# Kernel tuning notes

Measured on AMD Instinct MI355X. Metric: run time of the kernel, lower is better.

## Reference

```python
import jax, jax.numpy as jnp
import numpy as np

ROBOT_W = 1.0
PHASE_W = 1.0
COHER_W = 10.0
SPEED_W = 5.0
MAX_SPEED = 10.0
SMOOTH_VEL_W = 0.05
SMOOTH_ACC_W = 0.01

# illegal phase transitions {(0,2),(1,0),(2,0),(2,1)} as a 3x3 lookup table
_ILLEGAL = np.zeros((3, 3), dtype=bool)
for a, b in [(0, 2), (1, 0), (2, 0), (2, 1)]:
    _ILLEGAL[a, b] = True
ILLEGAL_TABLE = jnp.asarray(_ILLEGAL)


def setup_inputs() -> dict:
    key = jax.random.key(0)
    k1, k2, k3, k4 = jax.random.split(key, 4)
    B, T = 256, 8192
    # scale by 8 so per-frame speeds (norm of diffs of 3-vectors) exceed MAX_SPEED
    pred_robot = jax.random.normal(k1, (B, T, 12), dtype=jnp.float32) * 8.0
    gt_robot = jax.random.normal(k2, (B, T, 12), dtype=jnp.float32) * 8.0
    pred_phase = jax.random.normal(k3, (B, T, 3), dtype=jnp.float32)
    gt_phase = jax.random.randint(k4, (B, T), 0, 3, dtype=jnp.int32)
    return {"pred_robot": pred_robot, "pred_phase": pred_phase,
            "gt_robot": gt_robot, "gt_phase": gt_phase}


def _coherence_loss(phase_logits):
    # vectorized replacement for the O(B*T) Python double loop
    p = jnp.argmax(phase_logits, axis=-1)            # [B, T]
    pt, pt1 = p[:, :-1], p[:, 1:]                    # [B, T-1]
    illegal = ILLEGAL_TABLE[pt, pt1]                 # [B, T-1] bool
    # logit of the (illegal) predicted phase at t+1
    sel = jnp.take_along_axis(phase_logits[:, 1:], pt1[..., None], axis=-1)[..., 0]
    loss_sum = jnp.sum(jnp.where(illegal, sel * sel, 0.0))
    count = jnp.sum(illegal)
    return jnp.where(count > 0, loss_sum / jnp.maximum(count, 1).astype(sel.dtype), 0.0)


def _speed_loss(pred_robot):
    B, T, D = pred_robot.shape
    vel = pred_robot[:, 1:] - pred_robot[:, :-1]     # [B, T-1, 12]
    pts = vel.reshape(B, T - 1, 4, 3)
    speeds = jnp.linalg.norm(pts, axis=-1)           # [B, T-1, 4]
    pen = jax.nn.relu(speeds - MAX_SPEED)
    return SPEED_W * jnp.mean(pen * pen)


def reference(pred_robot, pred_phase, gt_robot, gt_phase):
    # MSE over robot trajectory
    robot_loss = jnp.mean((pred_robot - gt_robot) ** 2)
    # cross-entropy over 3 phase classes
    logp = jax.nn.log_softmax(pred_phase, axis=-1)   # [B, T, 3]
    nll = -jnp.take_along_axis(logp, gt_phase[..., None].astype(jnp.int32), axis=-1)[..., 0]
    phase_loss = jnp.mean(nll)
    coherence = _coherence_loss(pred_phase)
    speed_loss = _speed_loss(pred_robot)
    vel = pred_robot[:, 1:] - pred_robot[:, :-1]
    vel_loss = jnp.mean(vel * vel)
    acc = pred_robot[:, 2:] - 2.0 * pred_robot[:, 1:-1] + pred_robot[:, :-2]
    acc_loss = jnp.mean(acc * acc)
    total = (ROBOT_W * robot_loss + PHASE_W * phase_loss + COHER_W * coherence
             + speed_loss + SMOOTH_VEL_W * vel_loss + SMOOTH_ACC_W * acc_loss)
    return total
```

## Files before the change

kernel.cpp:

```cpp
#include <hip/hip_runtime.h>
#include <math.h>

#define B_DIM 256
#define T_DIM 8192
#define BLOCK 256
#define ITERS 4
#define RB_BLOCKS 6144
#define PH_BLOCKS 1536
#define GRID_BLOCKS (RB_BLOCKS + PH_BLOCKS)
#define NSLOT 256
#define N4_ROBOT (B_DIM * T_DIM * 3)
#define N4_PHASE (B_DIM * T_DIM * 3 / 4)
#define BF4_ROBOT (T_DIM * 3)
#define BF4_PHASE (T_DIM * 3 / 4)


__global__ __launch_bounds__(BLOCK) void combined_loss_main(
    const float4* __restrict__ pred4,
    const float*  __restrict__ pred_phase,
    const float4* __restrict__ gt4,
    const int*    __restrict__ gt_phase,
    double* __restrict__ ws)
{
    __shared__ float s_red[4][8];
    const int tid = threadIdx.x;
    const int bx  = (int)blockIdx.x;

    float sse=0.f, nll=0.f, csum=0.f, ccnt=0.f, pen2=0.f, velsq=0.f, accsq=0.f;

    if (bx < RB_BLOCKS) {
        const int Jbase = bx * (BLOCK * ITERS);
        const int jbase = (bx % 24) * (BLOCK * ITERS);
        #pragma unroll
        for (int it = 0; it < ITERS; ++it) {
            const int o = it * BLOCK + tid;
            const int J = Jbase + o;
            const int j = jbase + o;

            float4 p0 = pred4[J];
            float4 g  = gt4[J];
            float4 p1 = pred4[min(J + 1, N4_ROBOT - 1)];
            float4 p3 = pred4[min(J + 3, N4_ROBOT - 1)];
            float4 p4 = pred4[min(J + 4, N4_ROBOT - 1)];
            float4 p6 = pred4[min(J + 6, N4_ROBOT - 1)];

            float d;
            d = p0.x - g.x; sse += d*d;  d = p0.y - g.y; sse += d*d;
            d = p0.z - g.z; sse += d*d;  d = p0.w - g.w; sse += d*d;

            const bool vv = j < (BF4_ROBOT - 3);
            const bool va = j < (BF4_ROBOT - 6);

            const float vx = p3.x - p0.x, vy = p3.y - p0.y;
            const float vz = p3.z - p0.z, vw = p3.w - p0.w;
            if (vv) velsq += vx*vx + vy*vy + vz*vz + vw*vw;

            if (va) {
                const float ax = p6.x - 2.f*p3.x + p0.x;
                const float ay = p6.y - 2.f*p3.y + p0.y;
                const float az = p6.z - 2.f*p3.z + p0.z;
                const float aw = p6.w - 2.f*p3.w + p0.w;
                accsq += ax*ax + ay*ay + az*az + aw*aw;
            }

            const float wx = p4.x - p1.x, wy = p4.y - p1.y;
            const int s3 = j % 3;
            const float c0x = (s3 == 0) ? vx : ((s3 == 1) ? vz : vy);
            const float c0y = (s3 == 0) ? vy : ((s3 == 1) ? vw : vz);
            const float c0z = (s3 == 0) ? vz : ((s3 == 1) ? wx : vw);
            if (vv) {
                const float sp0 = sqrtf(c0x*c0x + c0y*c0y + c0z*c0z);
                const float d0 = sp0 - 10.f;
                if (d0 > 0.f) pen2 += d0*d0;
                if (s3 == 0) {
                    const float sp1 = sqrtf(vw*vw + wx*wx + wy*wy);
                    const float d1 = sp1 - 10.f;
                    if (d1 > 0.f) pen2 += d1*d1;
                }
            }
        }
    } else {
        const int pb    = bx - RB_BLOCKS;
        const int batch = pb / 6;
        const int Mbase = pb * (BLOCK * ITERS);
        const int mbase = (pb % 6) * (BLOCK * ITERS);
        const int bT    = batch * T_DIM;
        const float4* ph4 = (const float4*)pred_phase;
        #pragma unroll
        for (int it = 0; it < ITERS; ++it) {
            const int o = it * BLOCK + tid;
            const int M = Mbase + o;
            const int m = mbase + o;

            float4 v  = ph4[M];
            float4 nv = ph4[min(M + 1, N4_PHASE - 1)];
            float4 nn = ph4[min(M + 2, N4_PHASE - 1)];

            const int q = m / 3;
            const int s = m - 3 * q;

            const int   rA  = 4*q + ((s == 0) ? 0 : ((s == 1) ? 2 : 3));
            const float la0 = (s == 0) ? v.x  : ((s == 1) ? v.z  : v.y);
            const float la1 = (s == 0) ? v.y  : ((s == 1) ? v.w  : v.z);
            const float la2 = (s == 0) ? v.z  : ((s == 1) ? nv.x : v.w);
            const float na0 = (s == 0) ? v.w  : ((s == 1) ? nv.y : nv.x);
            const float na1 = (s == 0) ? nv.x : ((s == 1) ? nv.z : nv.y);
            const float na2 = (s == 0) ? nv.y : ((s == 1) ? nv.w : nv.z);

            const int gA = gt_phase[bT + rA];
            {
                const float mx  = fmaxf(la0, fmaxf(la1, la2));
                const float lse = mx + logf(expf(la0-mx) + expf(la1-mx) + expf(la2-mx));
                const float sl  = (gA == 0) ? la0 : ((gA == 1) ? la1 : la2);
                nll += lse - sl;
            }
            if (rA < T_DIM - 1) {
                int p = 0; float pm = la0;
                if (la1 > pm) { pm = la1; p = 1; }
                if (la2 > pm) { pm = la2; p = 2; }
                int p1 = 0; float m1 = na0;
                if (na1 > m1) { m1 = na1; p1 = 1; }
                if (na2 > m1) { m1 = na2; p1 = 2; }
                const int mask = (p == 0) ? 4 : ((p == 1) ? 1 : 3);
                if ((mask >> p1) & 1) { csum += m1*m1; ccnt += 1.f; }
            }

            if (s == 0) {
                const int   rB  = 4*q + 1;
                const float lb0 = v.w,  lb1 = nv.x, lb2 = nv.y;
                const float nb0 = nv.z, nb1 = nv.w, nb2 = nn.x;
                const int gB = gt_phase[bT + rB];
                const float mx  = fmaxf(lb0, fmaxf(lb1, lb2));
                const float lse = mx + logf(expf(lb0-mx) + expf(lb1-mx) + expf(lb2-mx));
                const float sl  = (gB == 0) ? lb0 : ((gB == 1) ? lb1 : lb2);
                nll += lse - sl;
                int p = 0; float pm = lb0;
                if (lb1 > pm) { pm = lb1; p = 1; }
                if (lb2 > pm) { pm = lb2; p = 2; }
                int p1 = 0; float m1 = nb0;
                if (nb1 > m1) { m1 = nb1; p1 = 1; }
                if (nb2 > m1) { m1 = nb2; p1 = 2; }
                const int mask = (p == 0) ? 4 : ((p == 1) ? 1 : 3);
                if ((mask >> p1) & 1) { csum += m1*m1; ccnt += 1.f; }
            }
        }
    }

    float vals[7] = { sse, nll, csum, ccnt, pen2, velsq, accsq };
    #pragma unroll
    for (int off = 32; off > 0; off >>= 1) {
        #pragma unroll
        for (int q = 0; q < 7; ++q)
            vals[q] += __shfl_down(vals[q], off, 64);
    }
    const int wave = tid >> 6, lane = tid & 63;
    if (lane == 0) {
        #pragma unroll
        for (int q = 0; q < 7; ++q) s_red[wave][q] = vals[q];
    }
    __syncthreads();
    if (tid < 7) {
        double acc = (double)s_red[0][tid] + (double)s_red[1][tid]
                   + (double)s_red[2][tid] + (double)s_red[3][tid];
        atomicAdd(&ws[(size_t)(bx & (NSLOT - 1)) * 8 + tid], acc);
    }
}

__global__ __launch_bounds__(256) void combined_loss_final(
    const double* __restrict__ ws, float* __restrict__ out)
{
    __shared__ double sred[4][7];
    const int tid = threadIdx.x;
    double v[7];
    #pragma unroll
    for (int q = 0; q < 7; ++q) v[q] = ws[(size_t)tid * 8 + q];
    #pragma unroll
    for (int off = 32; off > 0; off >>= 1) {
        #pragma unroll
        for (int q = 0; q < 7; ++q)
            v[q] += __shfl_down(v[q], off, 64);
    }
    const int wave = tid >> 6, lane = tid & 63;
    if (lane == 0) {
        #pragma unroll
        for (int q = 0; q < 7; ++q) sred[wave][q] = v[q];
    }
    __syncthreads();
    if (tid == 0) {
        double s[7];
        #pragma unroll
        for (int q = 0; q < 7; ++q)
            s[q] = sred[0][q] + sred[1][q] + sred[2][q] + sred[3][q];
        const double robot = s[0] / (double)((size_t)B_DIM * T_DIM * 12);
        const double phase = s[1] / (double)((size_t)B_DIM * T_DIM);
        const double coher = (s[3] > 0.0) ? (s[2] / fmax(s[3], 1.0)) : 0.0;
        const double speed = 5.0  * (s[4] / (double)((size_t)B_DIM * (T_DIM - 1) * 4));
        const double vel   = 0.05 * (s[5] / (double)((size_t)B_DIM * (T_DIM - 1) * 12));
        const double acc   = 0.01 * (s[6] / (double)((size_t)B_DIM * (T_DIM - 2) * 12));
        out[0] = (float)(robot + phase + 10.0 * coher + speed + vel + acc);
    }
}

extern "C" void kernel_launch(void* const* d_in, const int* in_sizes, int n_in,
                              void* d_out, int out_size, void* d_ws, size_t ws_size,
                              hipStream_t stream)
{
    const float4* pred4      = (const float4*)d_in[0];
    const float*  pred_phase = (const float*)d_in[1];
    const float4* gt4        = (const float4*)d_in[2];
    const int*    gt_phase   = (const int*)d_in[3];
    double* ws  = (double*)d_ws;
    float*  out = (float*)d_out;

    hipMemsetAsync(d_ws, 0, (size_t)NSLOT * 8 * sizeof(double), stream);

    combined_loss_main<<<dim3(GRID_BLOCKS), BLOCK, 0, stream>>>(pred4, pred_phase, gt4, gt_phase, ws);
    combined_loss_final<<<1, 256, 0, stream>>>(ws, out);
}
```

Measured before the change: 241.1 us.

## Give each thread four contiguous float4s and reuse neighbor loads from registers

Each thread now handles four consecutive float4 elements instead of four elements strided by the block size. It loads a sliding window of 10 (robot) or 6 (phase) float4s once and reuses them across the four iterations, replacing 24 or 12 separate neighbor loads. The gt_phase loads are also hoisted ahead of the compute. The catch is that neighboring lanes now access addresses 64 bytes apart, so loads are no longer coalesced across a wavefront, and register pressure rises.

```diff
diff --git a/kernel.cpp b/kernel.cpp
--- a/kernel.cpp
+++ b/kernel.cpp
@@ -4,7 +4,6 @@
 #define B_DIM 256
 #define T_DIM 8192
 #define BLOCK 256
-#define ITERS 4
 #define RB_BLOCKS 6144
 #define PH_BLOCKS 1536
 #define GRID_BLOCKS (RB_BLOCKS + PH_BLOCKS)
@@ -12,7 +11,6 @@
 #define N4_ROBOT (B_DIM * T_DIM * 3)
 #define N4_PHASE (B_DIM * T_DIM * 3 / 4)
 #define BF4_ROBOT (T_DIM * 3)
-#define BF4_PHASE (T_DIM * 3 / 4)
 
 
 __global__ __launch_bounds__(BLOCK) void combined_loss_main(
@@ -29,20 +27,21 @@
     float sse=0.f, nll=0.f, csum=0.f, ccnt=0.f, pen2=0.f, velsq=0.f, accsq=0.f;
 
     if (bx < RB_BLOCKS) {
-        const int Jbase = bx * (BLOCK * ITERS);
-        const int jbase = (bx % 24) * (BLOCK * ITERS);
-        #pragma unroll
-        for (int it = 0; it < ITERS; ++it) {
-            const int o = it * BLOCK + tid;
-            const int J = Jbase + o;
-            const int j = jbase + o;
-
-            float4 p0 = pred4[J];
-            float4 g  = gt4[J];
-            float4 p1 = pred4[min(J + 1, N4_ROBOT - 1)];
-            float4 p3 = pred4[min(J + 3, N4_ROBOT - 1)];
-            float4 p4 = pred4[min(J + 4, N4_ROBOT - 1)];
-            float4 p6 = pred4[min(J + 6, N4_ROBOT - 1)];
+        const int J0 = bx * 1024 + tid * 4;
+        const int j0 = (bx % 24) * 1024 + tid * 4;
+
+        float4 A[10];
+        #pragma unroll
+        for (int k = 0; k < 10; ++k) A[k] = pred4[min(J0 + k, N4_ROBOT - 1)];
+        float4 G[4];
+        #pragma unroll
+        for (int k = 0; k < 4; ++k) G[k] = gt4[J0 + k];
+
+        #pragma unroll
+        for (int i = 0; i < 4; ++i) {
+            const float4 p0 = A[i], p3 = A[i+3], p6 = A[i+6], g = G[i];
+            const float4 p1 = A[i+1], p4 = A[i+4];
+            const int j = j0 + i;
 
             float d;
             d = p0.x - g.x; sse += d*d;  d = p0.y - g.y; sse += d*d;
@@ -82,24 +81,31 @@
     } else {
         const int pb    = bx - RB_BLOCKS;
         const int batch = pb / 6;
-        const int Mbase = pb * (BLOCK * ITERS);
-        const int mbase = (pb % 6) * (BLOCK * ITERS);
+        const int M0    = pb * 1024 + tid * 4;
+        const int m0    = (pb % 6) * 1024 + tid * 4;
         const int bT    = batch * T_DIM;
         const float4* ph4 = (const float4*)pred_phase;
-        #pragma unroll
-        for (int it = 0; it < ITERS; ++it) {
-            const int o = it * BLOCK + tid;
-            const int M = Mbase + o;
-            const int m = mbase + o;
-
-            float4 v  = ph4[M];
-            float4 nv = ph4[min(M + 1, N4_PHASE - 1)];
-            float4 nn = ph4[min(M + 2, N4_PHASE - 1)];
-
-            const int q = m / 3;
-            const int s = m - 3 * q;
-
-            const int   rA  = 4*q + ((s == 0) ? 0 : ((s == 1) ? 2 : 3));
+
+        float4 A[6];
+        #pragma unroll
+        for (int k = 0; k < 6; ++k) A[k] = ph4[min(M0 + k, N4_PHASE - 1)];
+
+        int qi[4], si[4], rA[4], gA[4], gB[4];
+        #pragma unroll
+        for (int i = 0; i < 4; ++i) {
+            const int m = m0 + i;
+            qi[i] = m / 3;
+            si[i] = m - 3 * qi[i];
+            rA[i] = 4*qi[i] + ((si[i] == 0) ? 0 : ((si[i] == 1) ? 2 : 3));
+            gA[i] = gt_phase[bT + rA[i]];
+            gB[i] = gt_phase[bT + 4*qi[i] + 1];
+        }
+
+        #pragma unroll
+        for (int i = 0; i < 4; ++i) {
+            const float4 v = A[i], nv = A[i+1], nn = A[i+2];
+            const int s = si[i];
+
             const float la0 = (s == 0) ? v.x  : ((s == 1) ? v.z  : v.y);
             const float la1 = (s == 0) ? v.y  : ((s == 1) ? v.w  : v.z);
             const float la2 = (s == 0) ? v.z  : ((s == 1) ? nv.x : v.w);
@@ -107,14 +113,13 @@
             const float na1 = (s == 0) ? nv.x : ((s == 1) ? nv.z : nv.y);
             const float na2 = (s == 0) ? nv.y : ((s == 1) ? nv.w : nv.z);
 
-            const int gA = gt_phase[bT + rA];
             {
                 const float mx  = fmaxf(la0, fmaxf(la1, la2));
                 const float lse = mx + logf(expf(la0-mx) + expf(la1-mx) + expf(la2-mx));
-                const float sl  = (gA == 0) ? la0 : ((gA == 1) ? la1 : la2);
+                const float sl  = (gA[i] == 0) ? la0 : ((gA[i] == 1) ? la1 : la2);
                 nll += lse - sl;
             }
-            if (rA < T_DIM - 1) {
+            if (rA[i] < T_DIM - 1) {
                 int p = 0; float pm = la0;
                 if (la1 > pm) { pm = la1; p = 1; }
                 if (la2 > pm) { pm = la2; p = 2; }
@@ -126,13 +131,11 @@
             }
 
             if (s == 0) {
-                const int   rB  = 4*q + 1;
                 const float lb0 = v.w,  lb1 = nv.x, lb2 = nv.y;
                 const float nb0 = nv.z, nb1 = nv.w, nb2 = nn.x;
-                const int gB = gt_phase[bT + rB];
                 const float mx  = fmaxf(lb0, fmaxf(lb1, lb2));
                 const float lse = mx + logf(expf(lb0-mx) + expf(lb1-mx) + expf(lb2-mx));
-                const float sl  = (gB == 0) ? lb0 : ((gB == 1) ? lb1 : lb2);
+                const float sl  = (gB[i] == 0) ? lb0 : ((gB[i] == 1) ? lb1 : lb2);
                 nll += lse - sl;
                 int p = 0; float pm = lb0;
                 if (lb1 > pm) { pm = lb1; p = 1; }
```

Result: no change. 242.1 us (+0.4%).
